# Performance work log

Measured on AMD Instinct MI355X. Metric: run time of the kernel, lower is better.

The kernel has to match this reference:

```python
import jax, jax.numpy as jnp
import numpy as np

DIM = 1024
HEADS = 16
DH = DIM // HEADS  # 64
DFF = 4096
EPS = 1e-5


def layer_norm(x, g, b):
    mu = jnp.mean(x, axis=-1, keepdims=True)
    var = jnp.mean(jnp.square(x - mu), axis=-1, keepdims=True)
    return (x - mu) * jax.lax.rsqrt(var + EPS) * g + b


def setup_inputs() -> dict:
    key = jax.random.key(0)
    ks = jax.random.split(key, 12)
    s = 0.02
    return {
        "encoder_input": jax.random.normal(ks[0], (4, 2048, DIM), jnp.float32),
        # per-head Q/K/V projections stacked over heads: [H, dim, d_head]
        "wq": jax.random.normal(ks[1], (HEADS, DIM, DH), jnp.float32) * s,
        "bq": jnp.zeros((HEADS, DH), jnp.float32),
        "wk": jax.random.normal(ks[2], (HEADS, DIM, DH), jnp.float32) * s,
        "bk": jnp.zeros((HEADS, DH), jnp.float32),
        "wv": jax.random.normal(ks[3], (HEADS, DIM, DH), jnp.float32) * s,
        "bv": jnp.zeros((HEADS, DH), jnp.float32),
        "ln1_g": jnp.ones((DIM,), jnp.float32),
        "ln1_b": jnp.zeros((DIM,), jnp.float32),
        "w1": jax.random.normal(ks[4], (DIM, DFF), jnp.float32) * s,
        "b1": jnp.zeros((DFF,), jnp.float32),
        "w2": jax.random.normal(ks[5], (DFF, DIM), jnp.float32) * s,
        "b2": jnp.zeros((DIM,), jnp.float32),
        "ln2_g": jnp.ones((DIM,), jnp.float32),
        "ln2_b": jnp.zeros((DIM,), jnp.float32),
    }


def reference(encoder_input, wq, bq, wk, bk, wv, bv, ln1_g, ln1_b,
              w1, b1, w2, b2, ln2_g, ln2_b):
    x = encoder_input  # [B, S, D]
    B, S, D = x.shape
    # per-head projections, batched over heads (same math as the head loop)
    q = jnp.einsum('bsd,hde->bhse', x, wq) + bq[None, :, None, :]
    k = jnp.einsum('bsd,hde->bhse', x, wk) + bk[None, :, None, :]
    v = jnp.einsum('bsd,hde->bhse', x, wv) + bv[None, :, None, :]
    scores = jnp.einsum('bhse,bhte->bhst', q, k) / jnp.sqrt(jnp.float32(DH))
    attn = jax.nn.softmax(scores, axis=-1)
    o = jnp.einsum('bhst,bhte->bhse', attn, v)  # [B, H, S, dh]
    self_attn = jnp.transpose(o, (0, 2, 1, 3)).reshape(B, S, D)  # concat heads on dim=2
    # residual: source + LayerNorm(target)  (dropout = identity in eval)
    res1 = x + layer_norm(self_attn, ln1_g, ln1_b)
    ff = jax.nn.relu(res1 @ w1 + b1) @ w2 + b2
    return res1 + layer_norm(ff, ln2_g, ln2_b)
```

## Files before the change

### kernel.cpp

```cpp
#include <hip/hip_runtime.h>
#include <cstdint>
#include <cmath>

typedef unsigned short u16;
using bf16x8 = __attribute__((ext_vector_type(8))) __bf16;
using f32x4  = __attribute__((ext_vector_type(4))) float;

#define MFMA(a, b, c) __builtin_amdgcn_mfma_f32_16x16x32_bf16((a), (b), (c), 0, 0, 0)

__device__ __forceinline__ float b2f(u16 u) {
    union { unsigned int i; float f; } x; x.i = ((unsigned int)u) << 16; return x.f;
}
__device__ __forceinline__ u16 f2b(float f) {
    union { float f; unsigned int i; } x; x.f = f;
    unsigned int r = x.i + 0x7FFFu + ((x.i >> 16) & 1u);
    return (u16)(r >> 16);
}
__device__ __forceinline__ u16 cvtb(float f) {
    __bf16 h = (__bf16)f;
    return *reinterpret_cast<u16*>(&h);
}
__device__ __forceinline__ uint32_t cvtpk(float lo, float hi) {
    uint32_t r;
    asm("v_cvt_pk_bf16_f32 %0, %1, %2" : "=v"(r) : "v"(lo), "v"(hi));
    return r;
}

__device__ __forceinline__ void gload16(const u16* g, u16* l) {
    __builtin_amdgcn_global_load_lds(
        (const __attribute__((address_space(1))) void*)g,
        (__attribute__((address_space(3))) void*)l, 16, 0, 0);
}

#define BAR do { asm volatile("" ::: "memory"); \
                 __builtin_amdgcn_s_barrier();  \
                 asm volatile("" ::: "memory"); } while (0)

__global__ __launch_bounds__(256) void xcvt_kernel(const float* __restrict__ X,
                                                   u16* __restrict__ Xb)
{
    size_t i = ((size_t)blockIdx.x * 256 + threadIdx.x) * 8;
    float4 a = *reinterpret_cast<const float4*>(&X[i]);
    float4 b = *reinterpret_cast<const float4*>(&X[i + 4]);
    ushort4 lo = {f2b(a.x), f2b(a.y), f2b(a.z), f2b(a.w)};
    ushort4 hi = {f2b(b.x), f2b(b.y), f2b(b.z), f2b(b.w)};
    *reinterpret_cast<ushort4*>(&Xb[i]) = lo;
    *reinterpret_cast<ushort4*>(&Xb[i + 4]) = hi;
}

__global__ __launch_bounds__(256) void wT_kernel(const float* __restrict__ W,
                                                 u16* __restrict__ Wt, int K, int N)
{
    __shared__ __align__(16) u16 Ts[64][72];
    const int k0 = blockIdx.x * 64, n0 = blockIdx.y * 64;
    const int tid = threadIdx.x;
    #pragma unroll
    for (int it = 0; it < 4; ++it) {
        int vI = tid + it * 256;
        int kr = vI >> 4, nc = (vI & 15) * 4;
        float4 f = *reinterpret_cast<const float4*>(&W[(size_t)(k0 + kr) * N + n0 + nc]);
        Ts[nc + 0][kr] = f2b(f.x);
        Ts[nc + 1][kr] = f2b(f.y);
        Ts[nc + 2][kr] = f2b(f.z);
        Ts[nc + 3][kr] = f2b(f.w);
    }
    __syncthreads();
    #pragma unroll
    for (int it = 0; it < 2; ++it) {
        int vI = tid + it * 256;
        int nr = vI >> 3, kc = (vI & 7) * 8;
        *reinterpret_cast<uint4*>(&Wt[(size_t)(n0 + nr) * K + k0 + kc]) =
            *reinterpret_cast<uint4*>(&Ts[nr][kc]);
    }
}

__global__ __launch_bounds__(256) void wqkvT_kernel(
    const float* __restrict__ Wq, const float* __restrict__ Wk,
    const float* __restrict__ Wv, u16* __restrict__ Wt)
{
    __shared__ __align__(16) u16 Ts[64][72];
    const int k0 = blockIdx.x * 64, h = blockIdx.y, m = blockIdx.z;
    const float* W = (m == 0 ? Wq : (m == 1 ? Wk : Wv)) + (size_t)h * 65536;
    const int tid = threadIdx.x;
    #pragma unroll
    for (int it = 0; it < 4; ++it) {
        int vI = tid + it * 256;
        int kr = vI >> 4, dc = (vI & 15) * 4;
        float4 f = *reinterpret_cast<const float4*>(&W[(size_t)(k0 + kr) * 64 + dc]);
        Ts[dc + 0][kr] = f2b(f.x);
        Ts[dc + 1][kr] = f2b(f.y);
        Ts[dc + 2][kr] = f2b(f.z);
        Ts[dc + 3][kr] = f2b(f.w);
    }
    __syncthreads();
    #pragma unroll
    for (int it = 0; it < 2; ++it) {
        int vI = tid + it * 256;
        int dr = vI >> 3, kc = (vI & 7) * 8;
        *reinterpret_cast<uint4*>(
            &Wt[((size_t)(m * 1024 + h * 64 + dr)) * 1024 + k0 + kc]) =
            *reinterpret_cast<uint4*>(&Ts[dr][kc]);
    }
}

__global__ __launch_bounds__(256) void biascat_kernel(
    const float* __restrict__ Bq, const float* __restrict__ Bk,
    const float* __restrict__ Bv, float* __restrict__ out)
{
    int i = blockIdx.x * 256 + threadIdx.x;
    const float* B = (i < 1024 ? Bq : (i < 2048 ? Bk : Bv));
    out[i] = B[i & 1023];
}

__device__ __forceinline__ void stage_half(const u16* __restrict__ gb, int K,
                                           u16* lr, int lane, int w)
{
    #pragma unroll
    for (int cc = 0; cc < 2; ++cc) {
        int c = w * 2 + cc;
        int l = c * 64 + lane;
        int lp = l ^ ((l >> 3) & 7);
        gload16(gb + (size_t)(lp >> 3) * K + (lp & 7) * 8, lr + c * 512);
    }
}

template <int RELU, int F32OUT>
__global__ __launch_bounds__(512, 2) void gemm8(
    const u16* __restrict__ A, const u16* __restrict__ Bt,
    const float* __restrict__ bias, void* __restrict__ Cv,
    int M, int N, int K)
{
    __shared__ __align__(16) u16 lds[65536];
    const int tid = threadIdx.x, lane = tid & 63, w = tid >> 6;
    const int wm = w >> 2, wn = w & 3;
    const int g = lane >> 4, ln = lane & 15;
    const int xr = (ln & 7) << 3;
    const int brow = (wn & 1) * 64;

    int nwg = gridDim.x * gridDim.y;
    int bid = blockIdx.y * gridDim.x + blockIdx.x;
    int swz = (bid & 7) * (nwg >> 3) + (bid >> 3);
    const int m0 = (swz % gridDim.x) * 256;
    const int n0 = (swz / gridDim.x) * 256;

    const u16* Ab = A + (size_t)m0 * K;
    const u16* Bb = Bt + (size_t)n0 * K;

    u16* ldsA[2] = { lds + wm * 8192,         lds + 32768 + wm * 8192 };
    u16* ldsB[2] = { lds + 16384 + (wn >> 1) * 8192,
                     lds + 49152 + (wn >> 1) * 8192 };

    f32x4 acc[8][4];
    #pragma unroll
    for (int i = 0; i < 8; ++i)
        #pragma unroll
        for (int j = 0; j < 4; ++j) acc[i][j] = (f32x4){0.f, 0.f, 0.f, 0.f};

    bf16x8 af[4][2], bf[2][2];

#define RD_A(d, mh)                                                           \
    _Pragma("unroll") for (int i = 0; i < 4; ++i)                             \
    _Pragma("unroll") for (int kk = 0; kk < 2; ++kk)                          \
        af[i][kk] = *(const bf16x8*)&ldsA[d][((mh)*64 + i*16 + ln)*64 +       \
                                             ((kk*32 + g*8) ^ xr)];
#define RD_B(d, nh)                                                           \
    _Pragma("unroll") for (int j = 0; j < 2; ++j)                             \
    _Pragma("unroll") for (int kk = 0; kk < 2; ++kk)                          \
        bf[j][kk] = *(const bf16x8*)&ldsB[d][(brow + (nh)*32 + j*16 + ln)*64  \
                                             + ((kk*32 + g*8) ^ xr)];
#define MMQ(mh, nh)                                                           \
    __builtin_amdgcn_s_setprio(1);                                            \
    _Pragma("unroll") for (int i = 0; i < 4; ++i)                             \
    _Pragma("unroll") for (int j = 0; j < 2; ++j) {                           \
        acc[(mh)*4+i][(nh)*2+j] =                                             \
            MFMA(af[i][0], bf[j][0], acc[(mh)*4+i][(nh)*2+j]);                \
        acc[(mh)*4+i][(nh)*2+j] =                                             \
            MFMA(af[i][1], bf[j][1], acc[(mh)*4+i][(nh)*2+j]);                \
    }                                                                         \
    __builtin_amdgcn_s_setprio(0);

    const int ntk = K >> 6;
    const int nit = ntk >> 1;

    stage_half(Ab,                           K, lds + 0,     lane, w);
    stage_half(Ab + (size_t)128 * K,         K, lds + 8192,  lane, w);
    stage_half(Bb,                           K, lds + 16384, lane, w);
    stage_half(Bb + (size_t)128 * K,         K, lds + 24576, lane, w);
    stage_half(Ab + 64,                      K, lds + 32768, lane, w);
    stage_half(Ab + (size_t)128 * K + 64,    K, lds + 40960, lane, w);
    asm volatile("s_waitcnt vmcnt(4)" ::: "memory");
    BAR;

    for (int u = 0; u < nit; ++u) {
        const int t1 = 2 * u + 1;
        int s0 = 2 * u + 2; if (s0 >= ntk) s0 = ntk - 1;
        int s1 = 2 * u + 3; if (s1 >= ntk) s1 = ntk - 1;
        RD_A(0, 0); RD_B(0, 0);
        stage_half(Bb + (size_t)t1 * 64, K, lds + 49152, lane, w);
        BAR; MMQ(0, 0); BAR;
        RD_B(0, 1);
        stage_half(Bb + (size_t)128 * K + (size_t)t1 * 64, K, lds + 57344, lane, w);
        BAR; MMQ(0, 1); BAR;
        RD_A(0, 1); RD_B(0, 0);
        BAR; MMQ(1, 0); BAR;
        RD_B(0, 1);
        stage_half(Ab + (size_t)s0 * 64, K, lds + 0, lane, w);
        BAR; MMQ(1, 1);
        asm volatile("s_waitcnt vmcnt(2)" ::: "memory");
        BAR;
        RD_A(1, 0); RD_B(1, 0);
        stage_half(Ab + (size_t)128 * K + (size_t)s0 * 64, K, lds + 8192, lane, w);
        BAR; MMQ(0, 0); BAR;
        RD_B(1, 1);
        stage_half(Bb + (size_t)s0 * 64, K, lds + 16384, lane, w);
        BAR; MMQ(0, 1); BAR;
        RD_A(1, 1); RD_B(1, 0);
        stage_half(Bb + (size_t)128 * K + (size_t)s0 * 64, K, lds + 24576, lane, w);
        BAR; MMQ(1, 0); BAR;
        RD_B(1, 1);
        stage_half(Ab + (size_t)s1 * 64, K, lds + 32768, lane, w);
        stage_half(Ab + (size_t)128 * K + (size_t)s1 * 64, K, lds + 40960, lane, w);
        BAR; MMQ(1, 1);
        asm volatile("s_waitcnt vmcnt(4)" ::: "memory");
        BAR;
    }
#undef RD_A
#undef RD_B
#undef MMQ

    asm volatile("s_waitcnt vmcnt(0)" ::: "memory");
    BAR;

    if (F32OUT) {
        float* C = (float*)Cv;
        float bv[4];
        #pragma unroll
        for (int j = 0; j < 4; ++j) bv[j] = bias[n0 + wn * 64 + j * 16 + ln];
        #pragma unroll
        for (int i = 0; i < 8; ++i)
            #pragma unroll
            for (int j = 0; j < 4; ++j)
                #pragma unroll
                for (int r = 0; r < 4; ++r) {
                    float v = acc[i][j][r] + bv[j];
                    if (RELU) v = fmaxf(v, 0.f);
                    int row = m0 + wm * 128 + i * 16 + g * 4 + r;
                    int col = n0 + wn * 64 + j * 16 + ln;
                    C[(size_t)row * N + col] = v;
                }
    } else {
        u16* C = (u16*)Cv;
        float bv[4];
        #pragma unroll
        for (int j = 0; j < 4; ++j) bv[j] = bias[n0 + wn * 64 + j * 16 + ln];
        #pragma unroll
        for (int i = 0; i < 8; ++i)
            #pragma unroll
            for (int j = 0; j < 4; ++j)
                #pragma unroll
                for (int r = 0; r < 4; ++r) {
                    float v = acc[i][j][r] + bv[j];
                    if (RELU) v = fmaxf(v, 0.f);
                    int row = wm * 128 + i * 16 + g * 4 + r;
                    int col = wn * 64 + j * 16 + ln;
                    lds[row * 256 + (col ^ ((row & 12) << 2))] = cvtb(v);
                }
        BAR;
        #pragma unroll
        for (int p = 0; p < 16; ++p) {
            int f = (p * 512 + tid) * 8;
            int row = f >> 8, col = f & 255;
            uint4 val = *(uint4*)&lds[row * 256 + (col ^ ((row & 12) << 2))];
            *(uint4*)&C[(size_t)(m0 + row) * N + n0 + col] = val;
        }
    }
}

template <int RELU, int F32OUT>
__global__ __launch_bounds__(512, 2) void gemm3(
    const u16* __restrict__ A, const u16* __restrict__ Bt,
    const float* __restrict__ bias, void* __restrict__ Cv,
    int M, int N, int K)
{
    __shared__ __align__(16) u16 lds[73728];
    const int tid = threadIdx.x, lane = tid & 63, w = tid >> 6;
    const int wm = w >> 2, wn = w & 3;
    const int g = lane >> 4, ln = lane & 15;
    const int xr = (ln & 7) << 3;
    const int bro = (wn & 1) * 64;

    int nwg = gridDim.x * gridDim.y;
    int bid = blockIdx.y * gridDim.x + blockIdx.x;
    int swz = (bid & 7) * (nwg >> 3) + (bid >> 3);
    const int m0 = (swz % gridDim.x) * 128;
    const int n0 = (swz / gridDim.x) * 256;

    const u16* Ab = A + (size_t)m0 * K;
    const u16* Bb = Bt + (size_t)n0 * K;

    f32x4 acc[4][4];
    #pragma unroll
    for (int i = 0; i < 4; ++i)
        #pragma unroll
        for (int j = 0; j < 4; ++j) acc[i][j] = (f32x4){0.f, 0.f, 0.f, 0.f};

    const int ntk = K >> 6;

    #pragma unroll
    for (int u = 0; u < 2; ++u) {
        stage_half(Ab + (size_t)u * 64, K, lds + u * 24576, lane, w);
        stage_half(Bb + (size_t)u * 64, K, lds + u * 24576 + 8192, lane, w);
        stage_half(Bb + (size_t)128 * K + (size_t)u * 64, K,
                   lds + u * 24576 + 16384, lane, w);
    }

    bf16x8 af[4][2], bf[2][2];

    for (int u = 0; u < ntk; ++u) {
        const int p = u % 3;
        if (u < ntk - 1) asm volatile("s_waitcnt vmcnt(6)" ::: "memory");
        else             asm volatile("s_waitcnt vmcnt(0)" ::: "memory");
        BAR;
        u16* bufA = lds + p * 24576;
        u16* bufB = lds + p * 24576 + 8192 + (wn >> 1) * 8192;
        const int us = u + 2;
        const int ps = us % 3;
        #pragma unroll
        for (int i = 0; i < 4; ++i)
            #pragma unroll
            for (int kk = 0; kk < 2; ++kk)
                af[i][kk] = *(const bf16x8*)&bufA[(wm * 64 + i * 16 + ln) * 64 +
                                                 ((kk * 32 + g * 8) ^ xr)];
        #pragma unroll
        for (int j = 0; j < 2; ++j)
            #pragma unroll
            for (int kk = 0; kk < 2; ++kk)
                bf[j][kk] = *(const bf16x8*)&bufB[(bro + j * 16 + ln) * 64 +
                                                  ((kk * 32 + g * 8) ^ xr)];
        if (us < ntk)
            stage_half(Ab + (size_t)us * 64, K, lds + ps * 24576, lane, w);
        __builtin_amdgcn_s_setprio(1);
        #pragma unroll
        for (int i = 0; i < 4; ++i)
            #pragma unroll
            for (int j = 0; j < 2; ++j) {
                acc[i][j] = MFMA(af[i][0], bf[j][0], acc[i][j]);
                acc[i][j] = MFMA(af[i][1], bf[j][1], acc[i][j]);
            }
        __builtin_amdgcn_s_setprio(0);
        #pragma unroll
        for (int j = 0; j < 2; ++j)
            #pragma unroll
            for (int kk = 0; kk < 2; ++kk)
                bf[j][kk] = *(const bf16x8*)&bufB[(bro + 32 + j * 16 + ln) * 64 +
                                                  ((kk * 32 + g * 8) ^ xr)];
        if (us < ntk) {
            stage_half(Bb + (size_t)us * 64, K, lds + ps * 24576 + 8192, lane, w);
            stage_half(Bb + (size_t)128 * K + (size_t)us * 64, K,
                       lds + ps * 24576 + 16384, lane, w);
        }
        __builtin_amdgcn_s_setprio(1);
        #pragma unroll
        for (int i = 0; i < 4; ++i)
            #pragma unroll
            for (int j = 0; j < 2; ++j) {
                acc[i][2 + j] = MFMA(af[i][0], bf[j][0], acc[i][2 + j]);
                acc[i][2 + j] = MFMA(af[i][1], bf[j][1], acc[i][2 + j]);
            }
        __builtin_amdgcn_s_setprio(0);
    }

    float bv[4];
    #pragma unroll
    for (int j = 0; j < 4; ++j) bv[j] = bias[n0 + wn * 64 + j * 16 + ln];

    if (F32OUT) {
        float* C = (float*)Cv;
        #pragma unroll
        for (int i = 0; i < 4; ++i)
            #pragma unroll
            for (int j = 0; j < 4; ++j)
                #pragma unroll
                for (int r = 0; r < 4; ++r) {
                    float v = acc[i][j][r] + bv[j];
                    if (RELU) v = fmaxf(v, 0.f);
                    int row = m0 + wm * 64 + i * 16 + g * 4 + r;
                    int col = n0 + wn * 64 + j * 16 + ln;
                    C[(size_t)row * N + col] = v;
                }
    } else {
        u16* C = (u16*)Cv;
        BAR;
        #pragma unroll
        for (int i = 0; i < 4; ++i)
            #pragma unroll
            for (int j = 0; j < 4; ++j)
                #pragma unroll
                for (int r = 0; r < 4; ++r) {
                    float v = acc[i][j][r] + bv[j];
                    if (RELU) v = fmaxf(v, 0.f);
                    int row = wm * 64 + i * 16 + g * 4 + r;
                    int col = wn * 64 + j * 16 + ln;
                    lds[row * 256 + (col ^ ((row & 12) << 2))] = cvtb(v);
                }
        BAR;
        #pragma unroll
        for (int p2 = 0; p2 < 8; ++p2) {
            int f = (p2 * 512 + tid) * 8;
            int row = f >> 8, col = f & 255;
            uint4 val = *(uint4*)&lds[row * 256 + (col ^ ((row & 12) << 2))];
            *(uint4*)&C[(size_t)(m0 + row) * N + n0 + col] = val;
        }
    }
}

__device__ __forceinline__ int sperm(int row) {
    return (row & 32) | ((row & 12) << 1) | ((row & 16) >> 2) | (row & 3);
}

__global__ __launch_bounds__(512, 4) void attn_kernel(
    const u16* __restrict__ QKV, u16* __restrict__ O)
{
    const int bh = blockIdx.x, b = bh >> 4, h = bh & 15;
    const int q0 = blockIdx.y * 256;
    const int tid = threadIdx.x;
    const int lane = tid & 63, w = tid >> 6;
    const int g = lane >> 4, ln = lane & 15;

    __shared__ __align__(16) u16 Ks[2][64][72];
    __shared__ __align__(16) u16 Vt2[2][64][72];

    const u16* Qp = QKV + (size_t)b * 2048 * 3072 + h * 64;
    const u16* Kp = Qp + 1024;
    const u16* Vp = Qp + 2048;

    bf16x8 qf[2][2];
    #pragma unroll
    for (int i = 0; i < 2; ++i)
        #pragma unroll
        for (int kk = 0; kk < 2; ++kk)
            qf[i][kk] = *reinterpret_cast<const bf16x8*>(
                &Qp[(size_t)(q0 + w * 32 + i * 16 + ln) * 3072 + kk * 32 + g * 8]);

    f32x4 oacc[2][4];
    #pragma unroll
    for (int i = 0; i < 2; ++i)
        #pragma unroll
        for (int n = 0; n < 4; ++n) oacc[i][n] = (f32x4){0.f, 0.f, 0.f, 0.f};
    float mrun[2] = {-1e30f, -1e30f};
    float lsum[2] = {0.f, 0.f};

    const float C1 = 0.125f * 1.44269504f;

    const int r0 = tid >> 3, c0 = (tid & 7) * 8;
    const int ss0 = sperm(r0) ^ c0;

    {
        uint4 ka = *reinterpret_cast<const uint4*>(&Kp[(size_t)r0 * 3072 + c0]);
        uint4 va = *reinterpret_cast<const uint4*>(&Vp[(size_t)r0 * 3072 + c0]);
        *reinterpret_cast<uint4*>(&Ks[0][r0][c0]) = ka;
        const u16* tva = reinterpret_cast<const u16*>(&va);
        #pragma unroll
        for (int j = 0; j < 8; ++j) Vt2[0][c0 + j][ss0] = tva[j];
    }
    __syncthreads();

    for (int t = 0; t < 32; ++t) {
        const int c = t & 1;
        uint4 ka, va;
        if (t < 31) {
            const size_t rb0 = (size_t)((t + 1) * 64 + r0) * 3072 + c0;
            ka = *reinterpret_cast<const uint4*>(&Kp[rb0]);
            va = *reinterpret_cast<const uint4*>(&Vp[rb0]);
        }

        f32x4 sc[4][2];
        #pragma unroll
        for (int j = 0; j < 4; ++j)
            #pragma unroll
            for (int i = 0; i < 2; ++i) sc[j][i] = (f32x4){0.f, 0.f, 0.f, 0.f};
        #pragma unroll
        for (int kk = 0; kk < 2; ++kk)
            #pragma unroll
            for (int j = 0; j < 4; ++j) {
                bf16x8 kf = *(const bf16x8*)&Ks[c][j * 16 + ln][kk * 32 + g * 8];
                sc[j][0] = MFMA(kf, qf[0][kk], sc[j][0]);
                sc[j][1] = MFMA(kf, qf[1][kk], sc[j][1]);
            }

        float tl[2];
        #pragma unroll
        for (int i = 0; i < 2; ++i) {
            float t01 = fmaxf(fmaxf(sc[0][i][0], sc[0][i][1]),
                              fmaxf(sc[0][i][2], sc[0][i][3]));
            float t23 = fmaxf(fmaxf(sc[1][i][0], sc[1][i][1]),
                              fmaxf(sc[1][i][2], sc[1][i][3]));
            float t45 = fmaxf(fmaxf(sc[2][i][0], sc[2][i][1]),
                              fmaxf(sc[2][i][2], sc[2][i][3]));
            float t67 = fmaxf(fmaxf(sc[3][i][0], sc[3][i][1]),
                              fmaxf(sc[3][i][2], sc[3][i][3]));
            tl[i] = fmaxf(fmaxf(t01, t23), fmaxf(t45, t67)) * C1;
        }
        int small_ = (tl[0] <= mrun[0] + 10.f) && (tl[1] <= mrun[1] + 10.f);
        if (!__all(small_)) {
            #pragma unroll
            for (int i = 0; i < 2; ++i) {
                float tt = tl[i];
                tt = fmaxf(tt, __shfl_xor(tt, 16));
                tt = fmaxf(tt, __shfl_xor(tt, 32));
                float mn = fmaxf(mrun[i], tt);
                float al = exp2f(mrun[i] - mn);
                mrun[i] = mn;
                lsum[i] *= al;
                #pragma unroll
                for (int r = 0; r < 4; ++r) {
                    float alr = __shfl(al, g * 4 + r);
                    #pragma unroll
                    for (int n = 0; n < 4; ++n) oacc[i][n][r] *= alr;
                }
            }
        }
        uint32_t pk[2][8];
        #pragma unroll
        for (int i = 0; i < 2; ++i) {
            float m_ = mrun[i];
            float ps = 0.f;
            #pragma unroll
            for (int j = 0; j < 4; ++j) {
                #pragma unroll
                for (int r = 0; r < 4; ++r) {
                    float p = exp2f(fmaf(sc[j][i][r], C1, -m_));
                    sc[j][i][r] = p;
                    ps += p;
                }
                pk[i][j * 2 + 0] = cvtpk(sc[j][i][0], sc[j][i][1]);
                pk[i][j * 2 + 1] = cvtpk(sc[j][i][2], sc[j][i][3]);
            }
            lsum[i] += ps;
        }

        #pragma unroll
        for (int kk = 0; kk < 2; ++kk) {
            union { uint32_t u[4]; bf16x8 v; } a0, a1;
            a0.u[0] = pk[0][kk * 4 + 0]; a0.u[1] = pk[0][kk * 4 + 1];
            a0.u[2] = pk[0][kk * 4 + 2]; a0.u[3] = pk[0][kk * 4 + 3];
            a1.u[0] = pk[1][kk * 4 + 0]; a1.u[1] = pk[1][kk * 4 + 1];
            a1.u[2] = pk[1][kk * 4 + 2]; a1.u[3] = pk[1][kk * 4 + 3];
            #pragma unroll
            for (int n = 0; n < 4; ++n) {
                int d = n * 16 + ln;
                bf16x8 vf = *(const bf16x8*)&Vt2[c][d][(kk * 32 + g * 8) ^ (d & 56)];
                oacc[0][n] = MFMA(a0.v, vf, oacc[0][n]);
                oacc[1][n] = MFMA(a1.v, vf, oacc[1][n]);
            }
        }

        if (t < 31) {
            *reinterpret_cast<uint4*>(&Ks[c ^ 1][r0][c0]) = ka;
            const u16* tva = reinterpret_cast<const u16*>(&va);
            #pragma unroll
            for (int j = 0; j < 8; ++j) Vt2[c ^ 1][c0 + j][ss0] = tva[j];
        }
        __syncthreads();
    }

    #pragma unroll
    for (int i = 0; i < 2; ++i) {
        float s = lsum[i];
        s += __shfl_xor(s, 16);
        s += __shfl_xor(s, 32);
        float rinv = __builtin_amdgcn_rcpf(s);
        #pragma unroll
        for (int r = 0; r < 4; ++r) {
            float rv = __shfl(rinv, g * 4 + r);
            int row = q0 + w * 32 + i * 16 + g * 4 + r;
            #pragma unroll
            for (int n = 0; n < 4; ++n)
                O[((size_t)(b * 2048 + row)) * 1024 + h * 64 + n * 16 + ln] =
                    cvtb(oacc[i][n][r] * rv);
        }
    }
}

template <int T_F32, int SRC_F32, int OUT_F32>
__global__ __launch_bounds__(256) void ln_add_kernel(
    const void* __restrict__ TV, const void* __restrict__ SrcV,
    const float* __restrict__ G, const float* __restrict__ Bt,
    void* __restrict__ OutV)
{
    const int row = blockIdx.x;
    const int tid = threadIdx.x;
    __shared__ float red[8];

    const size_t rb = (size_t)row * 1024;
    float v0, v1, v2, v3;
    if (T_F32) {
        float4 tv = *reinterpret_cast<const float4*>((const float*)TV + rb + tid * 4);
        v0 = tv.x; v1 = tv.y; v2 = tv.z; v3 = tv.w;
    } else {
        ushort4 tv = *reinterpret_cast<const ushort4*>((const u16*)TV + rb + tid * 4);
        v0 = b2f(tv.x); v1 = b2f(tv.y); v2 = b2f(tv.z); v3 = b2f(tv.w);
    }
    float s = v0 + v1 + v2 + v3;
    float sq = v0 * v0 + v1 * v1 + v2 * v2 + v3 * v3;
    #pragma unroll
    for (int mm = 1; mm < 64; mm <<= 1) {
        s += __shfl_xor(s, mm);
        sq += __shfl_xor(sq, mm);
    }
    if ((tid & 63) == 0) { red[tid >> 6] = s; red[4 + (tid >> 6)] = sq; }
    __syncthreads();
    s = red[0] + red[1] + red[2] + red[3];
    sq = red[4] + red[5] + red[6] + red[7];
    float mu = s * (1.f / 1024.f);
    float var = sq * (1.f / 1024.f) - mu * mu;
    float rs = rsqrtf(var + 1e-5f);

    float s0, s1, s2, s3;
    if (SRC_F32) {
        float4 sv = *reinterpret_cast<const float4*>((const float*)SrcV + rb + tid * 4);
        s0 = sv.x; s1 = sv.y; s2 = sv.z; s3 = sv.w;
    } else {
        ushort4 sv = *reinterpret_cast<const ushort4*>((const u16*)SrcV + rb + tid * 4);
        s0 = b2f(sv.x); s1 = b2f(sv.y); s2 = b2f(sv.z); s3 = b2f(sv.w);
    }
    float4 gv = *reinterpret_cast<const float4*>(&G[tid * 4]);
    float4 bv = *reinterpret_cast<const float4*>(&Bt[tid * 4]);
    float o0 = s0 + (v0 - mu) * rs * gv.x + bv.x;
    float o1 = s1 + (v1 - mu) * rs * gv.y + bv.y;
    float o2 = s2 + (v2 - mu) * rs * gv.z + bv.z;
    float o3 = s3 + (v3 - mu) * rs * gv.w + bv.w;
    if (OUT_F32) {
        float4 ov = {o0, o1, o2, o3};
        *reinterpret_cast<float4*>((float*)OutV + rb + tid * 4) = ov;
    } else {
        ushort4 ov = {f2b(o0), f2b(o1), f2b(o2), f2b(o3)};
        *reinterpret_cast<ushort4*>((u16*)OutV + rb + tid * 4) = ov;
    }
}

extern "C" void kernel_launch(void* const* d_in, const int* in_sizes, int n_in,
                              void* d_out, int out_size, void* d_ws, size_t ws_size,
                              hipStream_t stream)
{
    const float* X   = (const float*)d_in[0];
    const float* Wq  = (const float*)d_in[1];
    const float* Bq  = (const float*)d_in[2];
    const float* Wk  = (const float*)d_in[3];
    const float* Bk  = (const float*)d_in[4];
    const float* Wv  = (const float*)d_in[5];
    const float* Bv  = (const float*)d_in[6];
    const float* g1  = (const float*)d_in[7];
    const float* b1  = (const float*)d_in[8];
    const float* W1  = (const float*)d_in[9];
    const float* B1  = (const float*)d_in[10];
    const float* W2  = (const float*)d_in[11];
    const float* B2  = (const float*)d_in[12];
    const float* g2  = (const float*)d_in[13];
    const float* b2  = (const float*)d_in[14];
    float* out = (float*)d_out;

    char* ws = (char*)d_ws;
    const size_t MiB = 1048576;
    u16*   qkv   = (u16*)(ws);
    u16*   Xb    = (u16*)(ws + 48 * MiB);
    u16*   attnb = (u16*)(ws + 48 * MiB);
    u16*   wqkvt = (u16*)(ws + 64 * MiB);
    float* bcat  = (float*)(ws + 70 * MiB);
    u16*   res1  = (u16*)(ws + 64 * MiB);
    u16*   hid   = (u16*)(ws);
    u16*   w1t   = (u16*)(ws + 80 * MiB);
    u16*   w2t   = (u16*)(ws + 88 * MiB);

    xcvt_kernel<<<4096, 256, 0, stream>>>(X, Xb);
    wT_kernel<<<dim3(16, 64), 256, 0, stream>>>(W1, w1t, 1024, 4096);
    wT_kernel<<<dim3(64, 16), 256, 0, stream>>>(W2, w2t, 4096, 1024);
    wqkvT_kernel<<<dim3(16, 16, 3), 256, 0, stream>>>(Wq, Wk, Wv, wqkvt);
    biascat_kernel<<<12, 256, 0, stream>>>(Bq, Bk, Bv, bcat);

    gemm3<0, 0><<<dim3(64, 12), 512, 0, stream>>>(Xb, wqkvt, bcat, qkv, 8192, 3072, 1024);
    attn_kernel<<<dim3(64, 8), 512, 0, stream>>>(qkv, attnb);
    ln_add_kernel<0, 1, 0><<<8192, 256, 0, stream>>>(attnb, X, g1, b1, res1);

    gemm8<1, 0><<<dim3(32, 16), 512, 0, stream>>>(res1, w1t, B1, hid, 8192, 4096, 1024);
    gemm3<0, 1><<<dim3(64, 4), 512, 0, stream>>>(hid, w2t, B2, out, 8192, 1024, 4096);
    ln_add_kernel<1, 0, 1><<<8192, 256, 0, stream>>>(out, res1, g2, b2, out);
}
```

Baseline: 359.8 us.

## Halve attention query tile per block and stream K via direct global-to-LDS loads

The attention kernel now processes 128 query rows per block (16 per wave) instead of 256, doubling the grid and raising the launch-bounds occupancy target. This cuts per-thread accumulator and score registers. K tiles are now loaded with a direct global-to-LDS copy (gload16) into a flat, XOR-swizzled layout instead of going through registers. The trade-off is that each K/V tile is reloaded twice as often per query, and an explicit vmcnt wait is added before each barrier.

```diff
diff --git a/kernel.cpp b/kernel.cpp
--- a/kernel.cpp
+++ b/kernel.cpp
@@ -418,166 +418,146 @@
     return (row & 32) | ((row & 12) << 1) | ((row & 16) >> 2) | (row & 3);
 }
 
-__global__ __launch_bounds__(512, 4) void attn_kernel(
+__global__ __launch_bounds__(512, 8) void attn_kernel(
     const u16* __restrict__ QKV, u16* __restrict__ O)
 {
     const int bh = blockIdx.x, b = bh >> 4, h = bh & 15;
-    const int q0 = blockIdx.y * 256;
+    const int q0 = blockIdx.y * 128;
     const int tid = threadIdx.x;
     const int lane = tid & 63, w = tid >> 6;
     const int g = lane >> 4, ln = lane & 15;
-
-    __shared__ __align__(16) u16 Ks[2][64][72];
+    const int xr = (ln & 7) << 3;
+
+    __shared__ __align__(16) u16 Ks[2][4096];
     __shared__ __align__(16) u16 Vt2[2][64][72];
 
     const u16* Qp = QKV + (size_t)b * 2048 * 3072 + h * 64;
     const u16* Kp = Qp + 1024;
     const u16* Vp = Qp + 2048;
 
-    bf16x8 qf[2][2];
-    #pragma unroll
-    for (int i = 0; i < 2; ++i)
-        #pragma unroll
-        for (int kk = 0; kk < 2; ++kk)
-            qf[i][kk] = *reinterpret_cast<const bf16x8*>(
-                &Qp[(size_t)(q0 + w * 32 + i * 16 + ln) * 3072 + kk * 32 + g * 8]);
-
-    f32x4 oacc[2][4];
-    #pragma unroll
-    for (int i = 0; i < 2; ++i)
-        #pragma unroll
-        for (int n = 0; n < 4; ++n) oacc[i][n] = (f32x4){0.f, 0.f, 0.f, 0.f};
-    float mrun[2] = {-1e30f, -1e30f};
-    float lsum[2] = {0.f, 0.f};
+    bf16x8 qf[2];
+    #pragma unroll
+    for (int kk = 0; kk < 2; ++kk)
+        qf[kk] = *reinterpret_cast<const bf16x8*>(
+            &Qp[(size_t)(q0 + w * 16 + ln) * 3072 + kk * 32 + g * 8]);
+
+    f32x4 oacc[4];
+    #pragma unroll
+    for (int n = 0; n < 4; ++n) oacc[n] = (f32x4){0.f, 0.f, 0.f, 0.f};
+    float mrun = -1e30f;
+    float lsum = 0.f;
 
     const float C1 = 0.125f * 1.44269504f;
 
     const int r0 = tid >> 3, c0 = (tid & 7) * 8;
     const int ss0 = sperm(r0) ^ c0;
+    const int lp = tid ^ ((tid >> 3) & 7);
+    const u16* Ksrc = Kp + (size_t)(lp >> 3) * 3072 + (lp & 7) * 8;
 
     {
-        uint4 ka = *reinterpret_cast<const uint4*>(&Kp[(size_t)r0 * 3072 + c0]);
+        gload16(Ksrc, &Ks[0][tid * 8]);
         uint4 va = *reinterpret_cast<const uint4*>(&Vp[(size_t)r0 * 3072 + c0]);
-        *reinterpret_cast<uint4*>(&Ks[0][r0][c0]) = ka;
         const u16* tva = reinterpret_cast<const u16*>(&va);
         #pragma unroll
         for (int j = 0; j < 8; ++j) Vt2[0][c0 + j][ss0] = tva[j];
+        asm volatile("s_waitcnt vmcnt(0)" ::: "memory");
     }
     __syncthreads();
 
     for (int t = 0; t < 32; ++t) {
         const int c = t & 1;
-        uint4 ka, va;
+        uint4 va;
         if (t < 31) {
-            const size_t rb0 = (size_t)((t + 1) * 64 + r0) * 3072 + c0;
-            ka = *reinterpret_cast<const uint4*>(&Kp[rb0]);
-            va = *reinterpret_cast<const uint4*>(&Vp[rb0]);
-        }
-
-        f32x4 sc[4][2];
-        #pragma unroll
-        for (int j = 0; j < 4; ++j)
-            #pragma unroll
-            for (int i = 0; i < 2; ++i) sc[j][i] = (f32x4){0.f, 0.f, 0.f, 0.f};
+            gload16(Ksrc + (size_t)(t + 1) * 64 * 3072, &Ks[c ^ 1][tid * 8]);
+            va = *reinterpret_cast<const uint4*>(
+                &Vp[(size_t)((t + 1) * 64 + r0) * 3072 + c0]);
+        }
+
+        f32x4 sc[4];
+        #pragma unroll
+        for (int j = 0; j < 4; ++j) sc[j] = (f32x4){0.f, 0.f, 0.f, 0.f};
         #pragma unroll
         for (int kk = 0; kk < 2; ++kk)
             #pragma unroll
             for (int j = 0; j < 4; ++j) {
-                bf16x8 kf = *(const bf16x8*)&Ks[c][j * 16 + ln][kk * 32 + g * 8];
-                sc[j][0] = MFMA(kf, qf[0][kk], sc[j][0]);
-                sc[j][1] = MFMA(kf, qf[1][kk], sc[j][1]);
+                bf16x8 kf = *(const bf16x8*)&Ks[c][(j * 16 + ln) * 64 +
+                                                  ((kk * 32 + g * 8) ^ xr)];
+                sc[j] = MFMA(kf, qf[kk], sc[j]);
             }
 
-        float tl[2];
-        #pragma unroll
-        for (int i = 0; i < 2; ++i) {
-            float t01 = fmaxf(fmaxf(sc[0][i][0], sc[0][i][1]),
-                              fmaxf(sc[0][i][2], sc[0][i][3]));
-            float t23 = fmaxf(fmaxf(sc[1][i][0], sc[1][i][1]),
-                              fmaxf(sc[1][i][2], sc[1][i][3]));
-            float t45 = fmaxf(fmaxf(sc[2][i][0], sc[2][i][1]),
-                              fmaxf(sc[2][i][2], sc[2][i][3]));
-            float t67 = fmaxf(fmaxf(sc[3][i][0], sc[3][i][1]),
-                              fmaxf(sc[3][i][2], sc[3][i][3]));
-            tl[i] = fmaxf(fmaxf(t01, t23), fmaxf(t45, t67)) * C1;
-        }
-        int small_ = (tl[0] <= mrun[0] + 10.f) && (tl[1] <= mrun[1] + 10.f);
+        float t01 = fmaxf(fmaxf(sc[0][0], sc[0][1]), fmaxf(sc[0][2], sc[0][3]));
+        float t23 = fmaxf(fmaxf(sc[1][0], sc[1][1]), fmaxf(sc[1][2], sc[1][3]));
+        float t45 = fmaxf(fmaxf(sc[2][0], sc[2][1]), fmaxf(sc[2][2], sc[2][3]));
+        float t67 = fmaxf(fmaxf(sc[3][0], sc[3][1]), fmaxf(sc[3][2], sc[3][3]));
+        float tl = fmaxf(fmaxf(t01, t23), fmaxf(t45, t67)) * C1;
+        int small_ = (tl <= mrun + 10.f);
         if (!__all(small_)) {
-            #pragma unroll
-            for (int i = 0; i < 2; ++i) {
-                float tt = tl[i];
-                tt = fmaxf(tt, __shfl_xor(tt, 16));
-                tt = fmaxf(tt, __shfl_xor(tt, 32));
-                float mn = fmaxf(mrun[i], tt);
-                float al = exp2f(mrun[i] - mn);
-                mrun[i] = mn;
-                lsum[i] *= al;
+            float tt = tl;
+            tt = fmaxf(tt, __shfl_xor(tt, 16));
+            tt = fmaxf(tt, __shfl_xor(tt, 32));
+            float mn = fmaxf(mrun, tt);
+            float al = exp2f(mrun - mn);
+            mrun = mn;
+            lsum *= al;
+            #pragma unroll
+            for (int r = 0; r < 4; ++r) {
+                float alr = __shfl(al, g * 4 + r);
                 #pragma unroll
-                for (int r = 0; r < 4; ++r) {
-                    float alr = __shfl(al, g * 4 + r);
-                    #pragma unroll
-                    for (int n = 0; n < 4; ++n) oacc[i][n][r] *= alr;
-                }
+                for (int n = 0; n < 4; ++n) oacc[n][r] *= alr;
             }
         }
-        uint32_t pk[2][8];
-        #pragma unroll
-        for (int i = 0; i < 2; ++i) {
-            float m_ = mrun[i];
+        uint32_t pk[8];
+        {
             float ps = 0.f;
             #pragma unroll
             for (int j = 0; j < 4; ++j) {
                 #pragma unroll
                 for (int r = 0; r < 4; ++r) {
-                    float p = exp2f(fmaf(sc[j][i][r], C1, -m_));
-                    sc[j][i][r] = p;
+                    float p = exp2f(fmaf(sc[j][r], C1, -mrun));
+                    sc[j][r] = p;
                     ps += p;
                 }
-                pk[i][j * 2 + 0] = cvtpk(sc[j][i][0], sc[j][i][1]);
-                pk[i][j * 2 + 1] = cvtpk(sc[j][i][2], sc[j][i][3]);
+                pk[j * 2 + 0] = cvtpk(sc[j][0], sc[j][1]);
+                pk[j * 2 + 1] = cvtpk(sc[j][2], sc[j][3]);
             }
-            lsum[i] += ps;
+            lsum += ps;
         }
 
         #pragma unroll
         for (int kk = 0; kk < 2; ++kk) {
-            union { uint32_t u[4]; bf16x8 v; } a0, a1;
-            a0.u[0] = pk[0][kk * 4 + 0]; a0.u[1] = pk[0][kk * 4 + 1];
-            a0.u[2] = pk[0][kk * 4 + 2]; a0.u[3] = pk[0][kk * 4 + 3];
-            a1.u[0] = pk[1][kk * 4 + 0]; a1.u[1] = pk[1][kk * 4 + 1];
-            a1.u[2] = pk[1][kk * 4 + 2]; a1.u[3] = pk[1][kk * 4 + 3];
+            union { uint32_t u[4]; bf16x8 v; } a0;
+            a0.u[0] = pk[kk * 4 + 0]; a0.u[1] = pk[kk * 4 + 1];
+            a0.u[2] = pk[kk * 4 + 2]; a0.u[3] = pk[kk * 4 + 3];
             #pragma unroll
             for (int n = 0; n < 4; ++n) {
                 int d = n * 16 + ln;
                 bf16x8 vf = *(const bf16x8*)&Vt2[c][d][(kk * 32 + g * 8) ^ (d & 56)];
-                oacc[0][n] = MFMA(a0.v, vf, oacc[0][n]);
-                oacc[1][n] = MFMA(a1.v, vf, oacc[1][n]);
+                oacc[n] = MFMA(a0.v, vf, oacc[n]);
             }
         }
 
         if (t < 31) {
-            *reinterpret_cast<uint4*>(&Ks[c ^ 1][r0][c0]) = ka;
             const u16* tva = reinterpret_cast<const u16*>(&va);
             #pragma unroll
             for (int j = 0; j < 8; ++j) Vt2[c ^ 1][c0 + j][ss0] = tva[j];
         }
+        asm volatile("s_waitcnt vmcnt(0)" ::: "memory");
         __syncthreads();
     }
 
-    #pragma unroll
-    for (int i = 0; i < 2; ++i) {
-        float s = lsum[i];
+    {
+        float s = lsum;
         s += __shfl_xor(s, 16);
         s += __shfl_xor(s, 32);
         float rinv = __builtin_amdgcn_rcpf(s);
         #pragma unroll
         for (int r = 0; r < 4; ++r) {
             float rv = __shfl(rinv, g * 4 + r);
-            int row = q0 + w * 32 + i * 16 + g * 4 + r;
+            int row = q0 + w * 16 + g * 4 + r;
             #pragma unroll
             for (int n = 0; n < 4; ++n)
                 O[((size_t)(b * 2048 + row)) * 1024 + h * 64 + n * 16 + ln] =
-                    cvtb(oacc[i][n][r] * rv);
+                    cvtb(oacc[n][r] * rv);
         }
     }
 }
@@ -679,7 +659,7 @@
     biascat_kernel<<<12, 256, 0, stream>>>(Bq, Bk, Bv, bcat);
 
     gemm3<0, 0><<<dim3(64, 12), 512, 0, stream>>>(Xb, wqkvt, bcat, qkv, 8192, 3072, 1024);
-    attn_kernel<<<dim3(64, 8), 512, 0, stream>>>(qkv, attnb);
+    attn_kernel<<<dim3(64, 16), 512, 0, stream>>>(qkv, attnb);
     ln_add_kernel<0, 1, 0><<<8192, 256, 0, stream>>>(attnb, X, g1, b1, res1);
 
     gemm8<1, 0><<<dim3(32, 16), 512, 0, stream>>>(res1, w1t, B1, hid, 8192, 4096, 1024);
```

Result: slower. 380.1 us (+5.7%).
